# Kernel optimization log

Hardware: AMD Instinct MI355X
Metric: run time of the kernel (lower is better)

The kernel has to match this reference:

```python
import jax, jax.numpy as jnp
import numpy as np

B, N = 8, 2048
IN_F, MID1, HID, MID2, OUT_F = 128, 128, 128, 128, 128
BIG = 9e15  # matches torch's 9000000000000000.0 additive mask constant


def _linear_params(key, out_d, in_d):
    # torch Linear layout: W is [out, in]
    kw, kb = jax.random.split(key)
    w = jax.random.normal(kw, (out_d, in_d), jnp.float32) * (1.0 / np.sqrt(in_d))
    b = jax.random.normal(kb, (out_d,), jnp.float32) * 0.01
    return w, b


def setup_inputs() -> dict:
    key = jax.random.key(0)
    ks = jax.random.split(key, 16)
    h = jax.random.normal(ks[0], (B, N, IN_F), jnp.float32)
    adj = jax.random.randint(ks[1], (B, N, N), 0, 2).astype(jnp.float32)
    vae2_fetures = jax.random.normal(ks[2], (B, N, OUT_F), jnp.float32)
    Wv1, bv1 = _linear_params(ks[3], MID1, IN_F)
    Wk1, bk1 = _linear_params(ks[4], MID1, IN_F)
    Wq1, bq1 = _linear_params(ks[5], MID1, IN_F)
    Wo1, bo1 = _linear_params(ks[6], HID, MID1)
    Wv2, bv2 = _linear_params(ks[7], MID2, HID)
    Wk2, bk2 = _linear_params(ks[8], MID2, HID)
    Wq2, bq2 = _linear_params(ks[9], MID2, HID)
    Wo2, bo2 = _linear_params(ks[10], OUT_F, MID2)
    Wf, bf = _linear_params(ks[11], OUT_F, 2 * OUT_F)
    return {
        "h": h, "adj": adj, "vae2_fetures": vae2_fetures,
        "Wv1": Wv1, "bv1": bv1, "Wk1": Wk1, "bk1": bk1, "Wq1": Wq1, "bq1": bq1,
        "Wo1": Wo1, "bo1": bo1,
        "Wv2": Wv2, "bv2": bv2, "Wk2": Wk2, "bk2": bk2, "Wq2": Wq2, "bq2": bq2,
        "Wo2": Wo2, "bo2": bo2, "Wf": Wf, "bf": bf,
    }


def _lin(x, W, b):
    return jnp.einsum('bnd,od->bno', x, W) + b


def _masked_att_block(x, adj, Wq, bq, Wk, bk, Wv, bv):
    v = jax.nn.relu(_lin(x, Wv, bv))          # [B,N,D]
    q = jax.nn.relu(_lin(x, Wq, bq))          # [B,N,D]
    k = jax.nn.relu(_lin(x, Wk, bk))          # [B,N,D]
    s = jnp.einsum('bnd,bmd->bnm', q, k)       # [B,N,N]
    masked = s * adj - BIG * (1.0 - adj)       # multiplicative + additive mask
    att = jax.nn.softmax(masked, axis=-1)
    return jnp.einsum('bnm,bmd->bnd', att, v)


def reference(h, adj, vae2_fetures,
              Wv1, bv1, Wk1, bk1, Wq1, bq1, Wo1, bo1,
              Wv2, bv2, Wk2, bk2, Wq2, bq2, Wo2, bo2,
              Wf, bf):
    f1 = _masked_att_block(h, adj, Wq1, bq1, Wk1, bk1, Wv1, bv1)
    f1 = _lin(f1, Wo1, bo1)                    # [B,N,HID]
    f2 = _masked_att_block(f1, adj, Wq2, bq2, Wk2, bk2, Wv2, bv2)
    f2 = _lin(f2, Wo2, bo2)                    # [B,N,OUT_F]
    f3 = jnp.concatenate([f2, vae2_fetures], axis=2)
    return _lin(f3, Wf, bf)                    # [B,N,OUT_F]
```

## Files before the change

kernel.cpp:

```cpp
#include <hip/hip_runtime.h>

typedef short s16x8 __attribute__((ext_vector_type(8)));
typedef float f32x4 __attribute__((ext_vector_type(4)));
typedef unsigned short u16x4v __attribute__((ext_vector_type(4)));

#define NSPLIT 4
#define NROWS 16384
#define MSHIFT 44.0f
#define NCH (2048 / NSPLIT / 64)

__device__ __forceinline__ unsigned short f2bf(float f) {
  union { float fl; unsigned int i; } v; v.fl = f;
  unsigned int x = v.i;
  x += 0x7fffu + ((x >> 16) & 1u);
  return (unsigned short)(x >> 16);
}
__device__ __forceinline__ s16x8 load8_bf16(const unsigned short* p) {
  return *(const s16x8*)p;
}
__device__ __forceinline__ s16x8 load8_f32(const float* p) {
  float4 a = *(const float4*)p;
  float4 b = *(const float4*)(p + 4);
  s16x8 r;
  r[0] = (short)f2bf(a.x); r[1] = (short)f2bf(a.y);
  r[2] = (short)f2bf(a.z); r[3] = (short)f2bf(a.w);
  r[4] = (short)f2bf(b.x); r[5] = (short)f2bf(b.y);
  r[6] = (short)f2bf(b.z); r[7] = (short)f2bf(b.w);
  return r;
}
__device__ __forceinline__ int vperm(int nn) {
  return (nn & ~31) | (((nn >> 2) & 3) << 3) | (((nn >> 4) & 1) << 2);
}

__device__ __forceinline__ void gload16(const void* g, void* l) {
  __builtin_amdgcn_global_load_lds(
      (const __attribute__((address_space(1))) void*)g,
      (__attribute__((address_space(3))) void*)l, 16, 0, 0);
}

template <int MODE>
__device__ __forceinline__ void qkv_body(
    const float* __restrict__ X, const float* __restrict__ W,
    const float* __restrict__ bias, unsigned short* __restrict__ out)
{
  const int t = threadIdx.x;
  const int w = t >> 6;
  const int lane = t & 63;
  const int l15 = lane & 15;
  const int quad = lane >> 4;
  const int mbase = blockIdx.x * 16;

  s16x8 a[4];
  const float* ar = X + (size_t)(mbase + l15) * 128;
#pragma unroll
  for (int ks = 0; ks < 4; ++ks) a[ks] = load8_f32(ar + ks * 32 + quad * 8);

#pragma unroll
  for (int nt = 0; nt < 2; ++nt) {
    const int n = (w * 2 + nt) * 16 + l15;
    f32x4 acc = {0.f, 0.f, 0.f, 0.f};
    const float* wr = W + (size_t)n * 128;
#pragma unroll
    for (int ks = 0; ks < 4; ++ks)
      acc = __builtin_amdgcn_mfma_f32_16x16x32_bf16(
          a[ks], load8_f32(wr + ks * 32 + quad * 8), acc, 0, 0, 0);
    const float bv = bias[n];
    if (MODE == 0) {
#pragma unroll
      for (int r = 0; r < 4; ++r)
        out[(size_t)(mbase + quad * 4 + r) * 128 + n] = f2bf(fmaxf(acc[r] + bv, 0.f));
    } else {
      const int b  = mbase >> 11;
      const int nn = (mbase & 2047) + quad * 4;
      u16x4v pk;
#pragma unroll
      for (int r = 0; r < 4; ++r) pk[r] = f2bf(fmaxf(acc[r] + bv, 0.f));
      *(u16x4v*)(out + (size_t)(b * 128 + n) * 2048 + vperm(nn)) = pk;
    }
  }
}

__global__ __launch_bounds__(256) void qkv1_kernel(
    const float* __restrict__ x,
    const float* __restrict__ Wq, const float* __restrict__ bq, unsigned short* __restrict__ oq,
    const float* __restrict__ Wk, const float* __restrict__ bk, unsigned short* __restrict__ ok,
    const float* __restrict__ Wv, const float* __restrict__ bv, unsigned short* __restrict__ ovt)
{
  if (blockIdx.y == 0)      qkv_body<0>(x, Wq, bq, oq);
  else if (blockIdx.y == 1) qkv_body<0>(x, Wk, bk, ok);
  else                      qkv_body<1>(x, Wv, bv, ovt);
}

template <bool PACK>
__global__ __launch_bounds__(256, 2) void attn_kernel(
    const unsigned short* __restrict__ Q,
    const unsigned short* __restrict__ K,
    const unsigned short* __restrict__ VT,
    const float* __restrict__ ADJ,
    unsigned long long* __restrict__ MASK,
    float* __restrict__ pO, float* __restrict__ pl)
{
  __shared__ __align__(16) unsigned short kbuf[2][64][128];
  __shared__ __align__(16) unsigned short vbuf[2][128][64];

  const int t = threadIdx.x;
  const int w = t >> 6;
  const int lane = t & 63;
  const int l15 = lane & 15;
  const int quad = lane >> 4;
  const int x7 = l15 & 7;

  const int gq0 = blockIdx.x * 128;
  const int b   = gq0 >> 11;
  const int wq0 = (gq0 & 2047) + w * 32;
  const int kc0 = blockIdx.y * (2048 / NSPLIT);

  const unsigned short* Kb  = K  + (size_t)(b * 2048) * 128;
  const unsigned short* VTb = VT + (size_t)(b * 128) * 2048;
  const float* ADJb = ADJ + (size_t)b * 2048 * 2048;
  unsigned long long* Mb = MASK + (size_t)b * 2048 * 32;

  const int krow = t >> 4;
  const int kc16 = t & 15;
  const int kchunk = kc16 ^ (krow & 7);
  const int vrow = t >> 3;
  const int vc16 = t & 7;
  const int vchunk = vc16 ^ (vrow & 7);

  s16x8 qf[2][4];
#pragma unroll
  for (int mt = 0; mt < 2; ++mt) {
    const unsigned short* qrow = Q + (size_t)(gq0 + w * 32 + mt * 16 + l15) * 128;
#pragma unroll
    for (int ks = 0; ks < 4; ++ks) qf[mt][ks] = load8_bf16(qrow + ks * 32 + quad * 8);
  }

  s16x8 ones;
#pragma unroll
  for (int i = 0; i < 8; ++i) ones[i] = (short)0x3F80;

  f32x4 accO[2][8];
  f32x4 accL[2];
#pragma unroll
  for (int mt = 0; mt < 2; ++mt) {
    accL[mt] = (f32x4){0.f, 0.f, 0.f, 0.f};
#pragma unroll
    for (int dt = 0; dt < 8; ++dt) accO[mt][dt] = (f32x4){0.f, 0.f, 0.f, 0.f};
  }

#pragma unroll
  for (int i = 0; i < 4; ++i)
    gload16(Kb + (size_t)(kc0 + i * 16 + krow) * 128 + kchunk * 8,
            &kbuf[0][i * 16 + krow][kc16 * 8]);
#pragma unroll
  for (int i = 0; i < 4; ++i)
    gload16(VTb + (size_t)(i * 32 + vrow) * 2048 + kc0 + vchunk * 8,
            &vbuf[0][i * 32 + vrow][vc16 * 8]);

  float4 a4c[2][4];
  unsigned long long mwc[2];
  if (PACK) {
#pragma unroll
    for (int mt = 0; mt < 2; ++mt)
#pragma unroll
      for (int nt = 0; nt < 4; ++nt)
        a4c[mt][nt] = *(const float4*)(
            ADJb + (size_t)(wq0 + mt * 16 + l15) * 2048 + kc0 + nt * 16 + quad * 4);
  } else {
#pragma unroll
    for (int mt = 0; mt < 2; ++mt)
      mwc[mt] = Mb[(size_t)(wq0 + mt * 16 + l15) * 32 + (kc0 >> 6)];
  }
  __syncthreads();

#pragma unroll 2
  for (int ci = 0; ci < NCH; ++ci) {
    const int kc = kc0 + ci * 64;
    unsigned short (*kb)[128] = kbuf[ci & 1];
    unsigned short (*vb)[64]  = vbuf[ci & 1];

    if (ci + 1 < NCH) {
      unsigned short (*kbn)[128] = kbuf[(ci + 1) & 1];
      unsigned short (*vbn)[64]  = vbuf[(ci + 1) & 1];
#pragma unroll
      for (int i = 0; i < 4; ++i)
        gload16(Kb + (size_t)(kc + 64 + i * 16 + krow) * 128 + kchunk * 8,
                &kbn[i * 16 + krow][kc16 * 8]);
#pragma unroll
      for (int i = 0; i < 4; ++i)
        gload16(VTb + (size_t)(i * 32 + vrow) * 2048 + (kc + 64) + vchunk * 8,
                &vbn[i * 32 + vrow][vc16 * 8]);
    }

    unsigned long long kept[2];
    if (PACK) {
#pragma unroll
      for (int mt = 0; mt < 2; ++mt) {
        unsigned long long word = 0;
#pragma unroll
        for (int nt = 0; nt < 4; ++nt) {
          unsigned int nib = 0;
          nib |= (a4c[mt][nt].x != 0.f) ? 1u : 0u;
          nib |= (a4c[mt][nt].y != 0.f) ? 2u : 0u;
          nib |= (a4c[mt][nt].z != 0.f) ? 4u : 0u;
          nib |= (a4c[mt][nt].w != 0.f) ? 8u : 0u;
          word |= (unsigned long long)nib << (nt * 16 + quad * 4);
        }
        kept[mt] = word;
      }
      if (ci + 1 < NCH) {
#pragma unroll
        for (int mt = 0; mt < 2; ++mt)
#pragma unroll
          for (int nt = 0; nt < 4; ++nt)
            a4c[mt][nt] = *(const float4*)(
                ADJb + (size_t)(wq0 + mt * 16 + l15) * 2048 + (kc + 64) + nt * 16 + quad * 4);
      }
    } else {
      kept[0] = mwc[0];
      kept[1] = mwc[1];
      if (ci + 1 < NCH) {
#pragma unroll
        for (int mt = 0; mt < 2; ++mt)
          mwc[mt] = Mb[(size_t)(wq0 + mt * 16 + l15) * 32 + ((kc + 64) >> 6)];
      }
    }

    f32x4 sv[2][4];
#pragma unroll
    for (int nt = 0; nt < 4; ++nt) {
      sv[0][nt] = (f32x4){0.f, 0.f, 0.f, 0.f};
      sv[1][nt] = (f32x4){0.f, 0.f, 0.f, 0.f};
    }
    __builtin_amdgcn_s_setprio(1);
#pragma unroll
    for (int nt = 0; nt < 4; ++nt)
#pragma unroll
      for (int ks = 0; ks < 4; ++ks) {
        s16x8 kf = *(const s16x8*)&kb[nt * 16 + l15][((ks * 4 + quad) ^ x7) * 8];
        sv[0][nt] = __builtin_amdgcn_mfma_f32_16x16x32_bf16(kf, qf[0][ks], sv[0][nt], 0, 0, 0);
        sv[1][nt] = __builtin_amdgcn_mfma_f32_16x16x32_bf16(kf, qf[1][ks], sv[1][nt], 0, 0, 0);
      }
    __builtin_amdgcn_s_setprio(0);

    s16x8 pf[2][2];
#pragma unroll
    for (int mt = 0; mt < 2; ++mt) {
      const unsigned int bl = (unsigned int)(kept[mt] >> (quad * 4));
      const unsigned int bh = (unsigned int)(kept[mt] >> (quad * 4 + 32));
#pragma unroll
      for (int ks = 0; ks < 2; ++ks) {
        s16x8 v;
#pragma unroll
        for (int half = 0; half < 2; ++half) {
          const int nt = ks * 2 + half;
          const unsigned int bits = (nt < 2) ? bl : bh;
          const int sh = (nt & 1) * 16;
#pragma unroll
          for (int r = 0; r < 4; ++r) {
            const float e = __expf(sv[mt][nt][r] - MSHIFT);
            const bool keep = (bits >> (sh + r)) & 1u;
            v[half * 4 + r] = (short)f2bf(keep ? e : 0.f);
          }
        }
        pf[mt][ks] = v;
      }
    }

    if (PACK) {
#pragma unroll
      for (int mt = 0; mt < 2; ++mt) {
        unsigned long long word = kept[mt];
        word |= __shfl_xor(word, 16, 64);
        word |= __shfl_xor(word, 32, 64);
        if (quad == 0)
          Mb[(size_t)(wq0 + mt * 16 + l15) * 32 + (kc >> 6)] = word;
      }
    }

    __builtin_amdgcn_s_setprio(1);
#pragma unroll
    for (int mt = 0; mt < 2; ++mt)
#pragma unroll
      for (int ks = 0; ks < 2; ++ks)
        accL[mt] = __builtin_amdgcn_mfma_f32_16x16x32_bf16(ones, pf[mt][ks], accL[mt], 0, 0, 0);

#pragma unroll
    for (int dt = 0; dt < 8; ++dt)
#pragma unroll
      for (int ks = 0; ks < 2; ++ks) {
        s16x8 vf = *(const s16x8*)&vb[dt * 16 + l15][((ks * 4 + quad) ^ x7) * 8];
        accO[0][dt] = __builtin_amdgcn_mfma_f32_16x16x32_bf16(vf, pf[0][ks], accO[0][dt], 0, 0, 0);
        accO[1][dt] = __builtin_amdgcn_mfma_f32_16x16x32_bf16(vf, pf[1][ks], accO[1][dt], 0, 0, 0);
      }
    __builtin_amdgcn_s_setprio(0);

    __syncthreads();
  }

  float* pOs = pO + (size_t)blockIdx.y * NROWS * 128;
#pragma unroll
  for (int mt = 0; mt < 2; ++mt) {
    const int qg = gq0 + w * 32 + mt * 16 + l15;
#pragma unroll
    for (int dt = 0; dt < 8; ++dt)
      *(f32x4*)(pOs + (size_t)qg * 128 + dt * 16 + quad * 4) = accO[mt][dt];
  }
  if (quad == 0) {
#pragma unroll
    for (int mt = 0; mt < 2; ++mt)
      pl[blockIdx.y * NROWS + gq0 + w * 32 + mt * 16 + l15] = accL[mt][0];
  }
}

__device__ __forceinline__ void combine_splits(
    const float* __restrict__ pO, const float* __restrict__ pl, int grow0,
    unsigned short (*At)[136])
{
  const int t = threadIdx.x;
  const int row = t >> 4;
  const int col8 = (t & 15) * 8;
  const int grow = grow0 + row;
  float lsum = 0.f;
#pragma unroll
  for (int s = 0; s < NSPLIT; ++s) lsum += pl[s * NROWS + grow];
  const float inv = (lsum > 0.f) ? 1.f / lsum : 0.f;
  float acc8[8];
#pragma unroll
  for (int i = 0; i < 8; ++i) acc8[i] = 0.f;
#pragma unroll
  for (int s = 0; s < NSPLIT; ++s) {
    const float* p = pO + (size_t)s * NROWS * 128 + (size_t)grow * 128 + col8;
    float4 x0 = *(const float4*)p;
    float4 x1 = *(const float4*)(p + 4);
    acc8[0] += x0.x; acc8[1] += x0.y; acc8[2] += x0.z; acc8[3] += x0.w;
    acc8[4] += x1.x; acc8[5] += x1.y; acc8[6] += x1.z; acc8[7] += x1.w;
  }
#pragma unroll
  for (int i = 0; i < 8; ++i) At[row][col8 + i] = f2bf(acc8[i] * inv);
}

__global__ __launch_bounds__(256) void redqkv_kernel(
    const float* __restrict__ pO, const float* __restrict__ pl,
    const float* __restrict__ Wo, const float* __restrict__ bo,
    const float* __restrict__ Wq, const float* __restrict__ bq, unsigned short* __restrict__ oq,
    const float* __restrict__ Wk, const float* __restrict__ bk, unsigned short* __restrict__ ok,
    const float* __restrict__ Wv, const float* __restrict__ bv, unsigned short* __restrict__ ovt)
{
  __shared__ __align__(16) unsigned short At[16][136];
  __shared__ __align__(16) unsigned short Bt[16][136];
  const int t = threadIdx.x;
  const int grow0 = blockIdx.x * 16;

  combine_splits(pO, pl, grow0, At);
  __syncthreads();

  const int w = t >> 6;
  const int lane = t & 63;
  const int l15 = lane & 15;
  const int quad = lane >> 4;

  s16x8 a[4];
#pragma unroll
  for (int ks = 0; ks < 4; ++ks) a[ks] = *(const s16x8*)&At[l15][ks * 32 + quad * 8];
#pragma unroll
  for (int nt = 0; nt < 2; ++nt) {
    const int n = (w * 2 + nt) * 16 + l15;
    f32x4 acc = {0.f, 0.f, 0.f, 0.f};
    const float* wr = Wo + (size_t)n * 128;
#pragma unroll
    for (int ks = 0; ks < 4; ++ks)
      acc = __builtin_amdgcn_mfma_f32_16x16x32_bf16(
          a[ks], load8_f32(wr + ks * 32 + quad * 8), acc, 0, 0, 0);
    const float bv_ = bo[n];
#pragma unroll
    for (int r = 0; r < 4; ++r) Bt[quad * 4 + r][n] = f2bf(acc[r] + bv_);
  }
  __syncthreads();

  s16x8 a2[4];
#pragma unroll
  for (int ks = 0; ks < 4; ++ks) a2[ks] = *(const s16x8*)&Bt[l15][ks * 32 + quad * 8];

#pragma unroll
  for (int which = 0; which < 3; ++which) {
    const float* W = (which == 0) ? Wq : (which == 1) ? Wk : Wv;
    const float* bb = (which == 0) ? bq : (which == 1) ? bk : bv;
    unsigned short* out = (which == 0) ? oq : (which == 1) ? ok : ovt;
#pragma unroll
    for (int nt = 0; nt < 2; ++nt) {
      const int n = (w * 2 + nt) * 16 + l15;
      f32x4 acc = {0.f, 0.f, 0.f, 0.f};
      const float* wr = W + (size_t)n * 128;
#pragma unroll
      for (int ks = 0; ks < 4; ++ks)
        acc = __builtin_amdgcn_mfma_f32_16x16x32_bf16(
            a2[ks], load8_f32(wr + ks * 32 + quad * 8), acc, 0, 0, 0);
      const float bv_ = bb[n];
      if (which < 2) {
#pragma unroll
        for (int r = 0; r < 4; ++r)
          out[(size_t)(grow0 + quad * 4 + r) * 128 + n] = f2bf(fmaxf(acc[r] + bv_, 0.f));
      } else {
        const int b  = grow0 >> 11;
        const int nn = (grow0 & 2047) + quad * 4;
        u16x4v pk;
#pragma unroll
        for (int r = 0; r < 4; ++r) pk[r] = f2bf(fmaxf(acc[r] + bv_, 0.f));
        *(u16x4v*)(out + (size_t)(b * 128 + n) * 2048 + vperm(nn)) = pk;
      }
    }
  }
}

__global__ __launch_bounds__(256) void redfinal_kernel(
    const float* __restrict__ pO, const float* __restrict__ pl,
    const float* __restrict__ Wo, const float* __restrict__ bo,
    const float* __restrict__ Wf, const float* __restrict__ bff,
    const float* __restrict__ vae2, float* __restrict__ out)
{
  __shared__ __align__(16) unsigned short At[16][136];
  __shared__ __align__(16) unsigned short Bt[16][136];
  const int t = threadIdx.x;
  const int grow0 = blockIdx.x * 16;

  combine_splits(pO, pl, grow0, At);
  __syncthreads();

  const int w = t >> 6;
  const int lane = t & 63;
  const int l15 = lane & 15;
  const int quad = lane >> 4;

  s16x8 a[4];
#pragma unroll
  for (int ks = 0; ks < 4; ++ks) a[ks] = *(const s16x8*)&At[l15][ks * 32 + quad * 8];
#pragma unroll
  for (int nt = 0; nt < 2; ++nt) {
    const int n = (w * 2 + nt) * 16 + l15;
    f32x4 acc = {0.f, 0.f, 0.f, 0.f};
    const float* wr = Wo + (size_t)n * 128;
#pragma unroll
    for (int ks = 0; ks < 4; ++ks)
      acc = __builtin_amdgcn_mfma_f32_16x16x32_bf16(
          a[ks], load8_f32(wr + ks * 32 + quad * 8), acc, 0, 0, 0);
    const float bv_ = bo[n];
#pragma unroll
    for (int r = 0; r < 4; ++r) Bt[quad * 4 + r][n] = f2bf(acc[r] + bv_);
  }
  __syncthreads();

  s16x8 a1[4], a2[4];
#pragma unroll
  for (int ks = 0; ks < 4; ++ks) a1[ks] = *(const s16x8*)&Bt[l15][ks * 32 + quad * 8];
  const float* vrow = vae2 + (size_t)(grow0 + l15) * 128;
#pragma unroll
  for (int ks = 0; ks < 4; ++ks) a2[ks] = load8_f32(vrow + ks * 32 + quad * 8);
#pragma unroll
  for (int nt = 0; nt < 2; ++nt) {
    const int n = (w * 2 + nt) * 16 + l15;
    f32x4 acc = {0.f, 0.f, 0.f, 0.f};
    const float* wr = Wf + (size_t)n * 256;
#pragma unroll
    for (int ks = 0; ks < 4; ++ks)
      acc = __builtin_amdgcn_mfma_f32_16x16x32_bf16(
          a1[ks], load8_f32(wr + ks * 32 + quad * 8), acc, 0, 0, 0);
#pragma unroll
    for (int ks = 0; ks < 4; ++ks)
      acc = __builtin_amdgcn_mfma_f32_16x16x32_bf16(
          a2[ks], load8_f32(wr + 128 + ks * 32 + quad * 8), acc, 0, 0, 0);
    const float bv_ = bff[n];
#pragma unroll
    for (int r = 0; r < 4; ++r)
      out[(size_t)(grow0 + quad * 4 + r) * 128 + n] = acc[r] + bv_;
  }
}

extern "C" void kernel_launch(void* const* d_in, const int* in_sizes, int n_in,
                              void* d_out, int out_size, void* d_ws, size_t ws_size,
                              hipStream_t stream)
{
  const float* h    = (const float*)d_in[0];
  const float* adj  = (const float*)d_in[1];
  const float* vae2 = (const float*)d_in[2];
  const float* Wv1  = (const float*)d_in[3];
  const float* bv1  = (const float*)d_in[4];
  const float* Wk1  = (const float*)d_in[5];
  const float* bk1  = (const float*)d_in[6];
  const float* Wq1  = (const float*)d_in[7];
  const float* bq1  = (const float*)d_in[8];
  const float* Wo1  = (const float*)d_in[9];
  const float* bo1  = (const float*)d_in[10];
  const float* Wv2  = (const float*)d_in[11];
  const float* bv2  = (const float*)d_in[12];
  const float* Wk2  = (const float*)d_in[13];
  const float* bk2  = (const float*)d_in[14];
  const float* Wq2  = (const float*)d_in[15];
  const float* bq2  = (const float*)d_in[16];
  const float* Wo2  = (const float*)d_in[17];
  const float* bo2  = (const float*)d_in[18];
  const float* Wf   = (const float*)d_in[19];
  const float* bff  = (const float*)d_in[20];

  char* wsb = (char*)d_ws;
  const size_t MB = 1u << 20;
  unsigned short* s_q  = (unsigned short*)(wsb + 0 * MB);
  unsigned short* s_k  = (unsigned short*)(wsb + 4 * MB);
  unsigned short* s_vt = (unsigned short*)(wsb + 8 * MB);
  unsigned long long* maskp = (unsigned long long*)(wsb + 12 * MB);
  float* pO = (float*)(wsb + 16 * MB);
  float* pl = (float*)(wsb + 48 * MB);

  qkv1_kernel<<<dim3(1024, 3), dim3(256), 0, stream>>>(
      h, Wq1, bq1, s_q, Wk1, bk1, s_k, Wv1, bv1, s_vt);
  attn_kernel<true><<<dim3(128, NSPLIT), dim3(256), 0, stream>>>(
      s_q, s_k, s_vt, adj, maskp, pO, pl);
  redqkv_kernel<<<dim3(1024), dim3(256), 0, stream>>>(
      pO, pl, Wo1, bo1, Wq2, bq2, s_q, Wk2, bk2, s_k, Wv2, bv2, s_vt);
  attn_kernel<false><<<dim3(128, NSPLIT), dim3(256), 0, stream>>>(
      s_q, s_k, s_vt, nullptr, maskp, pO, pl);
  redfinal_kernel<<<dim3(1024), dim3(256), 0, stream>>>(
      pO, pl, Wo2, bo2, Wf, bff, vae2, (float*)d_out);
}
```

Baseline: 378.0 us.

## Pack adjacency bitmask in QKV kernel and enlarge reduce-kernel row tiles

```diff
diff --git a/kernel.cpp b/kernel.cpp
--- a/kernel.cpp
+++ b/kernel.cpp
@@ -38,10 +38,31 @@
       (__attribute__((address_space(3))) void*)l, 16, 0, 0);
 }
 
-template <int MODE>
-__device__ __forceinline__ void qkv_body(
-    const float* __restrict__ X, const float* __restrict__ W,
-    const float* __restrict__ bias, unsigned short* __restrict__ out)
+__device__ __forceinline__ void pack_adj_body(
+    const float* __restrict__ ADJ, unsigned long long* __restrict__ MASK)
+{
+  const int t = threadIdx.x;
+  const int w = t >> 6;
+  const int lane = t & 63;
+  const int row0 = blockIdx.x * 16 + w * 4;
+#pragma unroll
+  for (int rr = 0; rr < 4; ++rr) {
+    const float* src = ADJ + (size_t)(row0 + rr) * 2048;
+    unsigned long long* dst = MASK + (size_t)(row0 + rr) * 32;
+#pragma unroll 8
+    for (int p = 0; p < 32; ++p) {
+      const float v = src[p * 64 + lane];
+      const unsigned long long word = __ballot(v != 0.f);
+      if (lane == 0) dst[p] = word;
+    }
+  }
+}
+
+__device__ __forceinline__ void qkv_merged_body(
+    const float* __restrict__ X,
+    const float* __restrict__ Wq, const float* __restrict__ bq, unsigned short* __restrict__ oq,
+    const float* __restrict__ Wk, const float* __restrict__ bk, unsigned short* __restrict__ ok,
+    const float* __restrict__ Wv, const float* __restrict__ bv, unsigned short* __restrict__ ovt)
 {
   const int t = threadIdx.x;
   const int w = t >> 6;
@@ -55,27 +76,37 @@
 #pragma unroll
   for (int ks = 0; ks < 4; ++ks) a[ks] = load8_f32(ar + ks * 32 + quad * 8);
 
-#pragma unroll
-  for (int nt = 0; nt < 2; ++nt) {
-    const int n = (w * 2 + nt) * 16 + l15;
-    f32x4 acc = {0.f, 0.f, 0.f, 0.f};
-    const float* wr = W + (size_t)n * 128;
-#pragma unroll
-    for (int ks = 0; ks < 4; ++ks)
-      acc = __builtin_amdgcn_mfma_f32_16x16x32_bf16(
-          a[ks], load8_f32(wr + ks * 32 + quad * 8), acc, 0, 0, 0);
-    const float bv = bias[n];
-    if (MODE == 0) {
-#pragma unroll
-      for (int r = 0; r < 4; ++r)
-        out[(size_t)(mbase + quad * 4 + r) * 128 + n] = f2bf(fmaxf(acc[r] + bv, 0.f));
-    } else {
-      const int b  = mbase >> 11;
-      const int nn = (mbase & 2047) + quad * 4;
-      u16x4v pk;
-#pragma unroll
-      for (int r = 0; r < 4; ++r) pk[r] = f2bf(fmaxf(acc[r] + bv, 0.f));
-      *(u16x4v*)(out + (size_t)(b * 128 + n) * 2048 + vperm(nn)) = pk;
+  const float* Ws[3] = {Wq, Wk, Wv};
+  const float* bs[3] = {bq, bk, bv};
+  unsigned short* outs[3] = {oq, ok, ovt};
+
+#pragma unroll
+  for (int which = 0; which < 3; ++which) {
+    const float* W = Ws[which];
+    const float* bias = bs[which];
+    unsigned short* out = outs[which];
+#pragma unroll
+    for (int nt = 0; nt < 2; ++nt) {
+      const int n = (w * 2 + nt) * 16 + l15;
+      f32x4 acc = {0.f, 0.f, 0.f, 0.f};
+      const float* wr = W + (size_t)n * 128;
+#pragma unroll
+      for (int ks = 0; ks < 4; ++ks)
+        acc = __builtin_amdgcn_mfma_f32_16x16x32_bf16(
+            a[ks], load8_f32(wr + ks * 32 + quad * 8), acc, 0, 0, 0);
+      const float bv_ = bias[n];
+      if (which < 2) {
+#pragma unroll
+        for (int r = 0; r < 4; ++r)
+          out[(size_t)(mbase + quad * 4 + r) * 128 + n] = f2bf(fmaxf(acc[r] + bv_, 0.f));
+      } else {
+        const int b  = mbase >> 11;
+        const int nn = (mbase & 2047) + quad * 4;
+        u16x4v pk;
+#pragma unroll
+        for (int r = 0; r < 4; ++r) pk[r] = f2bf(fmaxf(acc[r] + bv_, 0.f));
+        *(u16x4v*)(out + (size_t)(b * 128 + n) * 2048 + vperm(nn)) = pk;
+      }
     }
   }
 }
@@ -84,20 +115,18 @@
     const float* __restrict__ x,
     const float* __restrict__ Wq, const float* __restrict__ bq, unsigned short* __restrict__ oq,
     const float* __restrict__ Wk, const float* __restrict__ bk, unsigned short* __restrict__ ok,
-    const float* __restrict__ Wv, const float* __restrict__ bv, unsigned short* __restrict__ ovt)
-{
-  if (blockIdx.y == 0)      qkv_body<0>(x, Wq, bq, oq);
-  else if (blockIdx.y == 1) qkv_body<0>(x, Wk, bk, ok);
-  else                      qkv_body<1>(x, Wv, bv, ovt);
-}
-
-template <bool PACK>
+    const float* __restrict__ Wv, const float* __restrict__ bv, unsigned short* __restrict__ ovt,
+    const float* __restrict__ adj, unsigned long long* __restrict__ mask)
+{
+  if (blockIdx.y == 0) qkv_merged_body(x, Wq, bq, oq, Wk, bk, ok, Wv, bv, ovt);
+  else                 pack_adj_body(adj, mask);
+}
+
 __global__ __launch_bounds__(256, 2) void attn_kernel(
     const unsigned short* __restrict__ Q,
     const unsigned short* __restrict__ K,
     const unsigned short* __restrict__ VT,
-    const float* __restrict__ ADJ,
-    unsigned long long* __restrict__ MASK,
+    const unsigned long long* __restrict__ MASK,
     float* __restrict__ pO, float* __restrict__ pl)
 {
   __shared__ __align__(16) unsigned short kbuf[2][64][128];
@@ -117,8 +146,7 @@
 
   const unsigned short* Kb  = K  + (size_t)(b * 2048) * 128;
   const unsigned short* VTb = VT + (size_t)(b * 128) * 2048;
-  const float* ADJb = ADJ + (size_t)b * 2048 * 2048;
-  unsigned long long* Mb = MASK + (size_t)b * 2048 * 32;
+  const unsigned long long* Mb = MASK + (size_t)b * 2048 * 32;
 
   const int krow = t >> 4;
   const int kc16 = t & 15;
@@ -157,20 +185,11 @@
     gload16(VTb + (size_t)(i * 32 + vrow) * 2048 + kc0 + vchunk * 8,
             &vbuf[0][i * 32 + vrow][vc16 * 8]);
 
-  float4 a4c[2][4];
   unsigned long long mwc[2];
-  if (PACK) {
-#pragma unroll
-    for (int mt = 0; mt < 2; ++mt)
-#pragma unroll
-      for (int nt = 0; nt < 4; ++nt)
-        a4c[mt][nt] = *(const float4*)(
-            ADJb + (size_t)(wq0 + mt * 16 + l15) * 2048 + kc0 + nt * 16 + quad * 4);
-  } else {
-#pragma unroll
-    for (int mt = 0; mt < 2; ++mt)
-      mwc[mt] = Mb[(size_t)(wq0 + mt * 16 + l15) * 32 + (kc0 >> 6)];
-  }
+#pragma unroll
+  for (int mt = 0; mt < 2; ++mt)
+    mwc[mt] = Mb[(size_t)(wq0 + mt * 16 + l15) * 32 + (kc0 >> 6)];
+
   __syncthreads();
 
 #pragma unroll 2
@@ -193,37 +212,12 @@
     }
 
     unsigned long long kept[2];
-    if (PACK) {
-#pragma unroll
-      for (int mt = 0; mt < 2; ++mt) {
-        unsigned long long word = 0;
-#pragma unroll
-        for (int nt = 0; nt < 4; ++nt) {
-          unsigned int nib = 0;
-          nib |= (a4c[mt][nt].x != 0.f) ? 1u : 0u;
-          nib |= (a4c[mt][nt].y != 0.f) ? 2u : 0u;
-          nib |= (a4c[mt][nt].z != 0.f) ? 4u : 0u;
-          nib |= (a4c[mt][nt].w != 0.f) ? 8u : 0u;
-          word |= (unsigned long long)nib << (nt * 16 + quad * 4);
-        }
-        kept[mt] = word;
-      }
-      if (ci + 1 < NCH) {
-#pragma unroll
-        for (int mt = 0; mt < 2; ++mt)
-#pragma unroll
-          for (int nt = 0; nt < 4; ++nt)
-            a4c[mt][nt] = *(const float4*)(
-                ADJb + (size_t)(wq0 + mt * 16 + l15) * 2048 + (kc + 64) + nt * 16 + quad * 4);
-      }
-    } else {
-      kept[0] = mwc[0];
-      kept[1] = mwc[1];
-      if (ci + 1 < NCH) {
-#pragma unroll
-        for (int mt = 0; mt < 2; ++mt)
-          mwc[mt] = Mb[(size_t)(wq0 + mt * 16 + l15) * 32 + ((kc + 64) >> 6)];
-      }
+    kept[0] = mwc[0];
+    kept[1] = mwc[1];
+    if (ci + 1 < NCH) {
+#pragma unroll
+      for (int mt = 0; mt < 2; ++mt)
+        mwc[mt] = Mb[(size_t)(wq0 + mt * 16 + l15) * 32 + ((kc + 64) >> 6)];
     }
 
     f32x4 sv[2][4];
@@ -267,17 +261,6 @@
       }
     }
 
-    if (PACK) {
-#pragma unroll
-      for (int mt = 0; mt < 2; ++mt) {
-        unsigned long long word = kept[mt];
-        word |= __shfl_xor(word, 16, 64);
-        word |= __shfl_xor(word, 32, 64);
-        if (quad == 0)
-          Mb[(size_t)(wq0 + mt * 16 + l15) * 32 + (kc >> 6)] = word;
-      }
-    }
-
     __builtin_amdgcn_s_setprio(1);
 #pragma unroll
     for (int mt = 0; mt < 2; ++mt)
@@ -313,31 +296,35 @@
   }
 }
 
-__device__ __forceinline__ void combine_splits(
+__device__ __forceinline__ void combine64(
     const float* __restrict__ pO, const float* __restrict__ pl, int grow0,
     unsigned short (*At)[136])
 {
   const int t = threadIdx.x;
-  const int row = t >> 4;
-  const int col8 = (t & 15) * 8;
-  const int grow = grow0 + row;
-  float lsum = 0.f;
-#pragma unroll
-  for (int s = 0; s < NSPLIT; ++s) lsum += pl[s * NROWS + grow];
-  const float inv = (lsum > 0.f) ? 1.f / lsum : 0.f;
-  float acc8[8];
-#pragma unroll
-  for (int i = 0; i < 8; ++i) acc8[i] = 0.f;
-#pragma unroll
-  for (int s = 0; s < NSPLIT; ++s) {
-    const float* p = pO + (size_t)s * NROWS * 128 + (size_t)grow * 128 + col8;
-    float4 x0 = *(const float4*)p;
-    float4 x1 = *(const float4*)(p + 4);
-    acc8[0] += x0.x; acc8[1] += x0.y; acc8[2] += x0.z; acc8[3] += x0.w;
-    acc8[4] += x1.x; acc8[5] += x1.y; acc8[6] += x1.z; acc8[7] += x1.w;
-  }
-#pragma unroll
-  for (int i = 0; i < 8; ++i) At[row][col8 + i] = f2bf(acc8[i] * inv);
+#pragma unroll
+  for (int u = 0; u < 4; ++u) {
+    const int unit = u * 256 + t;
+    const int row = unit >> 4;
+    const int col8 = (unit & 15) * 8;
+    const int grow = grow0 + row;
+    float lsum = 0.f;
+#pragma unroll
+    for (int s = 0; s < NSPLIT; ++s) lsum += pl[s * NROWS + grow];
+    const float inv = (lsum > 0.f) ? 1.f / lsum : 0.f;
+    float acc8[8];
+#pragma unroll
+    for (int i = 0; i < 8; ++i) acc8[i] = 0.f;
+#pragma unroll
+    for (int s = 0; s < NSPLIT; ++s) {
+      const float* p = pO + (size_t)s * NROWS * 128 + (size_t)grow * 128 + col8;
+      float4 x0 = *(const float4*)p;
+      float4 x1 = *(const float4*)(p + 4);
+      acc8[0] += x0.x; acc8[1] += x0.y; acc8[2] += x0.z; acc8[3] += x0.w;
+      acc8[4] += x1.x; acc8[5] += x1.y; acc8[6] += x1.z; acc8[7] += x1.w;
+    }
+#pragma unroll
+    for (int i = 0; i < 8; ++i) At[row][col8 + i] = f2bf(acc8[i] * inv);
+  }
 }
 
 __global__ __launch_bounds__(256) void redqkv_kernel(
@@ -347,12 +334,12 @@
     const float* __restrict__ Wk, const float* __restrict__ bk, unsigned short* __restrict__ ok,
     const float* __restrict__ Wv, const float* __restrict__ bv, unsigned short* __restrict__ ovt)
 {
-  __shared__ __align__(16) unsigned short At[16][136];
-  __shared__ __align__(16) unsigned short Bt[16][136];
+  __shared__ __align__(16) unsigned short At[64][136];
+  __shared__ __align__(16) unsigned short Bt[64][136];
   const int t = threadIdx.x;
-  const int grow0 = blockIdx.x * 16;
-
-  combine_splits(pO, pl, grow0, At);
+  const int grow0 = blockIdx.x * 64;
+
+  combine64(pO, pl, grow0, At);
   __syncthreads();
 
   const int w = t >> 6;
@@ -360,27 +347,43 @@
   const int l15 = lane & 15;
   const int quad = lane >> 4;
 
-  s16x8 a[4];
-#pragma unroll
-  for (int ks = 0; ks < 4; ++ks) a[ks] = *(const s16x8*)&At[l15][ks * 32 + quad * 8];
+  s16x8 af[4][4];
+#pragma unroll
+  for (int mt = 0; mt < 4; ++mt)
+#pragma unroll
+    for (int ks = 0; ks < 4; ++ks)
+      af[mt][ks] = *(const s16x8*)&At[mt * 16 + l15][ks * 32 + quad * 8];
+
 #pragma unroll
   for (int nt = 0; nt < 2; ++nt) {
     const int n = (w * 2 + nt) * 16 + l15;
-    f32x4 acc = {0.f, 0.f, 0.f, 0.f};
     const float* wr = Wo + (size_t)n * 128;
+    s16x8 wf[4];
+#pragma unroll
+    for (int ks = 0; ks < 4; ++ks) wf[ks] = load8_f32(wr + ks * 32 + quad * 8);
+    f32x4 acc[4];
+#pragma unroll
+    for (int mt = 0; mt < 4; ++mt) acc[mt] = (f32x4){0.f, 0.f, 0.f, 0.f};
+#pragma unroll
+    for (int mt = 0; mt < 4; ++mt)
+#pragma unroll
+      for (int ks = 0; ks < 4; ++ks)
+        acc[mt] = __builtin_amdgcn_mfma_f32_16x16x32_bf16(af[mt][ks], wf[ks], acc[mt], 0, 0, 0);
+    const float bv_ = bo[n];
+#pragma unroll
+    for (int mt = 0; mt < 4; ++mt)
+#pragma unroll
+      for (int r = 0; r < 4; ++r)
+        Bt[mt * 16 + quad * 4 + r][n] = f2bf(acc[mt][r] + bv_);
+  }
+  __syncthreads();
+
+  s16x8 a2[4][4];
+#pragma unroll
+  for (int mt = 0; mt < 4; ++mt)
 #pragma unroll
     for (int ks = 0; ks < 4; ++ks)
-      acc = __builtin_amdgcn_mfma_f32_16x16x32_bf16(
-          a[ks], load8_f32(wr + ks * 32 + quad * 8), acc, 0, 0, 0);
-    const float bv_ = bo[n];
-#pragma unroll
-    for (int r = 0; r < 4; ++r) Bt[quad * 4 + r][n] = f2bf(acc[r] + bv_);
-  }
-  __syncthreads();
-
-  s16x8 a2[4];
-#pragma unroll
-  for (int ks = 0; ks < 4; ++ks) a2[ks] = *(const s16x8*)&Bt[l15][ks * 32 + quad * 8];
+      a2[mt][ks] = *(const s16x8*)&Bt[mt * 16 + l15][ks * 32 + quad * 8];
 
 #pragma unroll
   for (int which = 0; which < 3; ++which) {
@@ -390,24 +393,36 @@
 #pragma unroll
     for (int nt = 0; nt < 2; ++nt) {
       const int n = (w * 2 + nt) * 16 + l15;
-      f32x4 acc = {0.f, 0.f, 0.f, 0.f};
       const float* wr = W + (size_t)n * 128;
-#pragma unroll
-      for (int ks = 0; ks < 4; ++ks)
-        acc = __builtin_amdgcn_mfma_f32_16x16x32_bf16(
-            a2[ks], load8_f32(wr + ks * 32 + quad * 8), acc, 0, 0, 0);
+      s16x8 wf[4];
+#pragma unroll
+      for (int ks = 0; ks < 4; ++ks) wf[ks] = load8_f32(wr + ks * 32 + quad * 8);
+      f32x4 acc[4];
+#pragma unroll
+      for (int mt = 0; mt < 4; ++mt) acc[mt] = (f32x4){0.f, 0.f, 0.f, 0.f};
+#pragma unroll
+      for (int mt = 0; mt < 4; ++mt)
+#pragma unroll
+        for (int ks = 0; ks < 4; ++ks)
+          acc[mt] = __builtin_amdgcn_mfma_f32_16x16x32_bf16(a2[mt][ks], wf[ks], acc[mt], 0, 0, 0);
       const float bv_ = bb[n];
       if (which < 2) {
 #pragma unroll
-        for (int r = 0; r < 4; ++r)
-          out[(size_t)(grow0 + quad * 4 + r) * 128 + n] = f2bf(fmaxf(acc[r] + bv_, 0.f));
+        for (int mt = 0; mt < 4; ++mt)
+#pragma unroll
+          for (int r = 0; r < 4; ++r)
+            out[(size_t)(grow0 + mt * 16 + quad * 4 + r) * 128 + n] =
+                f2bf(fmaxf(acc[mt][r] + bv_, 0.f));
       } else {
-        const int b  = grow0 >> 11;
-        const int nn = (grow0 & 2047) + quad * 4;
-        u16x4v pk;
-#pragma unroll
-        for (int r = 0; r < 4; ++r) pk[r] = f2bf(fmaxf(acc[r] + bv_, 0.f));
-        *(u16x4v*)(out + (size_t)(b * 128 + n) * 2048 + vperm(nn)) = pk;
+        const int b = grow0 >> 11;
+#pragma unroll
+        for (int mt = 0; mt < 4; ++mt) {
+          const int nn = (grow0 & 2047) + mt * 16 + quad * 4;
+          u16x4v pk;
+#pragma unroll
+          for (int r = 0; r < 4; ++r) pk[r] = f2bf(fmaxf(acc[mt][r] + bv_, 0.f));
+          *(u16x4v*)(out + (size_t)(b * 128 + n) * 2048 + vperm(nn)) = pk;
+        }
       }
     }
   }
@@ -419,12 +434,12 @@
     const float* __restrict__ Wf, const float* __restrict__ bff,
     const float* __restrict__ vae2, float* __restrict__ out)
 {
-  __shared__ __align__(16) unsigned short At[16][136];
-  __shared__ __align__(16) unsigned short Bt[16][136];
+  __shared__ __align__(16) unsigned short At[64][136];
+  __shared__ __align__(16) unsigned short Bt[64][136];
   const int t = threadIdx.x;
-  const int grow0 = blockIdx.x * 16;
-
-  combine_splits(pO, pl, grow0, At);
+  const int grow0 = blockIdx.x * 64;
+
+  combine64(pO, pl, grow0, At);
   __syncthreads();
 
   const int w = t >> 6;
@@ -432,47 +447,76 @@
   const int l15 = lane & 15;
   const int quad = lane >> 4;
 
-  s16x8 a[4];
-#pragma unroll
-  for (int ks = 0; ks < 4; ++ks) a[ks] = *(const s16x8*)&At[l15][ks * 32 + quad * 8];
+  s16x8 af[4][4];
+#pragma unroll
+  for (int mt = 0; mt < 4; ++mt)
+#pragma unroll
+    for (int ks = 0; ks < 4; ++ks)
+      af[mt][ks] = *(const s16x8*)&At[mt * 16 + l15][ks * 32 + quad * 8];
+
 #pragma unroll
   for (int nt = 0; nt < 2; ++nt) {
     const int n = (w * 2 + nt) * 16 + l15;
-    f32x4 acc = {0.f, 0.f, 0.f, 0.f};
     const float* wr = Wo + (size_t)n * 128;
+    s16x8 wf[4];
+#pragma unroll
+    for (int ks = 0; ks < 4; ++ks) wf[ks] = load8_f32(wr + ks * 32 + quad * 8);
+    f32x4 acc[4];
+#pragma unroll
+    for (int mt = 0; mt < 4; ++mt) acc[mt] = (f32x4){0.f, 0.f, 0.f, 0.f};
+#pragma unroll
+    for (int mt = 0; mt < 4; ++mt)
+#pragma unroll
+      for (int ks = 0; ks < 4; ++ks)
+        acc[mt] = __builtin_amdgcn_mfma_f32_16x16x32_bf16(af[mt][ks], wf[ks], acc[mt], 0, 0, 0);
+    const float bv_ = bo[n];
+#pragma unroll
+    for (int mt = 0; mt < 4; ++mt)
+#pragma unroll
+      for (int r = 0; r < 4; ++r)
+        Bt[mt * 16 + quad * 4 + r][n] = f2bf(acc[mt][r] + bv_);
+  }
+  __syncthreads();
+
+  s16x8 a1[4][4], a2[4][4];
+#pragma unroll
+  for (int mt = 0; mt < 4; ++mt) {
 #pragma unroll
     for (int ks = 0; ks < 4; ++ks)
-      acc = __builtin_amdgcn_mfma_f32_16x16x32_bf16(
-          a[ks], load8_f32(wr + ks * 32 + quad * 8), acc, 0, 0, 0);
-    const float bv_ = bo[n];
-#pragma unroll
-    for (int r = 0; r < 4; ++r) Bt[quad * 4 + r][n] = f2bf(acc[r] + bv_);
-  }
-  __syncthreads();
-
-  s16x8 a1[4], a2[4];
-#pragma unroll
-  for (int ks = 0; ks < 4; ++ks) a1[ks] = *(const s16x8*)&Bt[l15][ks * 32 + quad * 8];
-  const float* vrow = vae2 + (size_t)(grow0 + l15) * 128;
-#pragma unroll
-  for (int ks = 0; ks < 4; ++ks) a2[ks] = load8_f32(vrow + ks * 32 + quad * 8);
+      a1[mt][ks] = *(const s16x8*)&Bt[mt * 16 + l15][ks * 32 + quad * 8];
+    const float* vrow = vae2 + (size_t)(grow0 + mt * 16 + l15) * 128;
+#pragma unroll
+    for (int ks = 0; ks < 4; ++ks) a2[mt][ks] = load8_f32(vrow + ks * 32 + quad * 8);
+  }
+
 #pragma unroll
   for (int nt = 0; nt < 2; ++nt) {
     const int n = (w * 2 + nt) * 16 + l15;
-    f32x4 acc = {0.f, 0.f, 0.f, 0.f};
     const float* wr = Wf + (size_t)n * 256;
-#pragma unroll
-    for (int ks = 0; ks < 4; ++ks)
-      acc = __builtin_amdgcn_mfma_f32_16x16x32_bf16(
-          a1[ks], load8_f32(wr + ks * 32 + quad * 8), acc, 0, 0, 0);
-#pragma unroll
-    for (int ks = 0; ks < 4; ++ks)
-      acc = __builtin_amdgcn_mfma_f32_16x16x32_bf16(
-          a2[ks], load8_f32(wr + 128 + ks * 32 + quad * 8), acc, 0, 0, 0);
+    s16x8 wfl[4], wfr[4];
+#pragma unroll
+    for (int ks = 0; ks < 4; ++ks) {
+      wfl[ks] = load8_f32(wr + ks * 32 + quad * 8);
+      wfr[ks] = load8_f32(wr + 128 + ks * 32 + quad * 8);
+    }
+    f32x4 acc[4];
+#pragma unroll
+    for (int mt = 0; mt < 4; ++mt) acc[mt] = (f32x4){0.f, 0.f, 0.f, 0.f};
+#pragma unroll
+    for (int mt = 0; mt < 4; ++mt) {
+#pragma unroll
+      for (int ks = 0; ks < 4; ++ks)
+        acc[mt] = __builtin_amdgcn_mfma_f32_16x16x32_bf16(a1[mt][ks], wfl[ks], acc[mt], 0, 0, 0);
+#pragma unroll
+      for (int ks = 0; ks < 4; ++ks)
+        acc[mt] = __builtin_amdgcn_mfma_f32_16x16x32_bf16(a2[mt][ks], wfr[ks], acc[mt], 0, 0, 0);
+    }
     const float bv_ = bff[n];
 #pragma unroll
-    for (int r = 0; r < 4; ++r)
-      out[(size_t)(grow0 + quad * 4 + r) * 128 + n] = acc[r] + bv_;
+    for (int mt = 0; mt < 4; ++mt)
+#pragma unroll
+      for (int r = 0; r < 4; ++r)
+        out[(size_t)(grow0 + mt * 16 + quad * 4 + r) * 128 + n] = acc[mt][r] + bv_;
   }
 }
 
@@ -511,14 +555,14 @@
   float* pO = (float*)(wsb + 16 * MB);
   float* pl = (float*)(wsb + 48 * MB);
 
-  qkv1_kernel<<<dim3(1024, 3), dim3(256), 0, stream>>>(
-      h, Wq1, bq1, s_q, Wk1, bk1, s_k, Wv1, bv1, s_vt);
-  attn_kernel<true><<<dim3(128, NSPLIT), dim3(256), 0, stream>>>(
-      s_q, s_k, s_vt, adj, maskp, pO, pl);
-  redqkv_kernel<<<dim3(1024), dim3(256), 0, stream>>>(
+  qkv1_kernel<<<dim3(1024, 2), dim3(256), 0, stream>>>(
+      h, Wq1, bq1, s_q, Wk1, bk1, s_k, Wv1, bv1, s_vt, adj, maskp);
+  attn_kernel<<<dim3(128, NSPLIT), dim3(256), 0, stream>>>(
+      s_q, s_k, s_vt, maskp, pO, pl);
+  redqkv_kernel<<<dim3(256), dim3(256), 0, stream>>>(
       pO, pl, Wo1, bo1, Wq2, bq2, s_q, Wk2, bk2, s_k, Wv2, bv2, s_vt);
-  attn_kernel<false><<<dim3(128, NSPLIT), dim3(256), 0, stream>>>(
-      s_q, s_k, s_vt, nullptr, maskp, pO, pl);
-  redfinal_kernel<<<dim3(1024), dim3(256), 0, stream>>>(
+  attn_kernel<<<dim3(128, NSPLIT), dim3(256), 0, stream>>>(
+      s_q, s_k, s_vt, maskp, pO, pl);
+  redfinal_kernel<<<dim3(256), dim3(256), 0, stream>>>(
       pO, pl, Wo2, bo2, Wf, bff, vae2, (float*)d_out);
 }
```

After: 391.6 us. 1.04x slower.
